# Optimization experiments

Hardware: AMD Instinct MI355X
Metric: run time of the kernel (lower is better)

Reference implementation:

```python
import jax, jax.numpy as jnp
import numpy as np

# --- low precision float format: exp=5, man=2, subnormals, nearest-even ---
EXP, MAN = 5, 2
BIAS = 2 ** (EXP - 1) - 1          # 15
EMIN = 1 - BIAS                     # -14 (min normal exponent; clamping here gives subnormals)
MAXV = (2.0 - 2.0 ** (-MAN)) * 2.0 ** BIAS


def _q(x):
    """Round x to nearest FP(exp=5, man=2) value (subnormals, clipped at max)."""
    ax = jnp.abs(x)
    e = jnp.floor(jnp.log2(jnp.where(ax > 0, ax, 1.0)))
    e = jnp.maximum(e, EMIN)
    scale = jnp.exp2(e - MAN)
    q = jnp.round(x / scale) * scale   # jnp.round = half-to-even
    q = jnp.clip(q, -MAXV, MAXV)
    return jnp.where(ax > 0, q, x).astype(x.dtype)


# Quantizer: forward quantize, straight-through (quantized) backward
@jax.custom_vjp
def fq(x):
    return _q(x)

def _fq_fwd(x):
    return _q(x), None

def _fq_bwd(_, g):
    return (_q(g),)

fq.defvjp(_fq_fwd, _fq_bwd)


def conv_valid(x, w):
    return jax.lax.conv_general_dilated(
        x, w, window_strides=(1, 1), padding='VALID',
        dimension_numbers=('NCHW', 'OIHW', 'NCHW'))


def qconv(x, w):
    # QConv2d: input_quant, weight_quant, conv, output_quant
    return fq(conv_valid(fq(x), fq(w)))


def qlinear(x, W, b):
    # QLinear: input_quant, weight_quant (weights + bias), matmul, output_quant
    return fq(fq(x) @ fq(W).T + fq(b))


def batchnorm(x, gamma, beta, eps=1e-5):
    # training-mode BatchNorm2d over (N,H,W) per channel
    m = x.mean(axis=(0, 2, 3), keepdims=True)
    v = x.var(axis=(0, 2, 3), keepdims=True)
    return (x - m) * jax.lax.rsqrt(v + eps) * gamma[None, :, None, None] + beta[None, :, None, None]


def maxpool2(x):
    return jax.lax.reduce_window(x, -jnp.inf, jax.lax.max,
                                 (1, 1, 2, 2), (1, 1, 2, 2), 'VALID')


def setup_inputs() -> dict:
    key = jax.random.key(0)
    ks = jax.random.split(key, 12)
    B = 8192
    inp = {
        'x':   jax.random.normal(ks[0], (B, 1, 32, 32), jnp.float32),
        'w1':  jax.random.normal(ks[1], (6, 1, 5, 5), jnp.float32) * 0.2,
        'g1':  jnp.ones((6,), jnp.float32),
        'be1': jnp.zeros((6,), jnp.float32),
        'w2':  jax.random.normal(ks[2], (16, 6, 5, 5), jnp.float32) * 0.1,
        'g2':  jnp.ones((16,), jnp.float32),
        'be2': jnp.zeros((16,), jnp.float32),
        'fw1': jax.random.normal(ks[3], (120, 400), jnp.float32) * 0.05,
        'fb1': jnp.zeros((120,), jnp.float32),
        'fw2': jax.random.normal(ks[4], (84, 120), jnp.float32) * 0.09,
        'fb2': jnp.zeros((84,), jnp.float32),
        'fw3': jax.random.normal(ks[5], (10, 84), jnp.float32) * 0.1,
        'fb3': jnp.zeros((10,), jnp.float32),
    }
    return inp


def reference(x, w1, g1, be1, w2, g2, be2, fw1, fb1, fw2, fb2, fw3, fb3):
    x = fq(x)                                   # act_error_quant
    x = qconv(x, w1)                            # conv1 (no bias)
    x = batchnorm(x, g1, be1)                   # bn1
    x = fq(x)                                   # act_error_quant
    x = maxpool2(jax.nn.relu(x))                # relu + 2x2 maxpool -> [B,6,14,14]
    x = qconv(x, w2)                            # conv2 -> [B,16,10,10]
    x = batchnorm(x, g2, be2)                   # bn2
    x = fq(x)
    x = maxpool2(jax.nn.relu(x))                # -> [B,16,5,5]
    x = x.reshape(x.shape[0], -1)               # [B,400]
    x = jax.nn.relu(qlinear(x, fw1, fb1))       # fc1
    x = jax.nn.relu(qlinear(x, fw2, fb2))       # fc2
    x = qlinear(x, fw3, fb3)                    # fc3 -> [B,10]
    return x
```

## Files before the change

### kernel.cpp

```cpp
#include <hip/hip_runtime.h>
#include <hip/hip_bf16.h>


#define BATCH 8192

__device__ __forceinline__ double fq_d(double x) {
    long long b = __double_as_longlong(x);
    long long ab = b & 0x7fffffffffffffffLL;
    if (ab == 0) return x;
    double q;
    if (ab >= 0x3F10000000000000LL) {
        long long r = b + 0x0001FFFFFFFFFFFFLL + ((b >> 50) & 1LL);
        r &= 0xFFFC000000000000LL;
        q = __longlong_as_double(r);
        q = fmin(fmax(q, -57344.0), 57344.0);
    } else {
        q = rint(x * 65536.0) * 1.52587890625e-05;
    }
    return q;
}

__device__ __forceinline__ float fq_f(float x) {
    int b = __float_as_int(x);
    int ab = b & 0x7fffffff;
    if (ab == 0) return x;
    float q;
    if (ab >= 0x38800000) {
        int r = b + 0x000FFFFF + ((b >> 21) & 1);
        r &= 0xFFE00000;
        q = __int_as_float(r);
        q = fminf(fmaxf(q, -57344.0f), 57344.0f);
    } else {
        q = rintf(x * 65536.0f) * 1.52587890625e-05f;
    }
    return q;
}

__device__ __forceinline__ unsigned short bfbits(double q) {
    __hip_bfloat16 h = __float2bfloat16((float)q);
    return *(unsigned short*)&h;
}

__global__ void kprep(const float* __restrict__ w1, const float* __restrict__ w2,
                      const float* __restrict__ fb1, const float* __restrict__ fb2,
                      const float* __restrict__ fb3, const float* __restrict__ fw1,
                      const float* __restrict__ fw2, const float* __restrict__ fw3,
                      float* __restrict__ qw1, float* __restrict__ qw2,
                      float* __restrict__ qfb1, float* __restrict__ qfb2,
                      float* __restrict__ qfb3, float* __restrict__ Wt1,
                      float* __restrict__ Wt2, float* __restrict__ Wt3) {
    int i = blockIdx.x * 256 + threadIdx.x;
    if (i < 150) { qw1[i] = fq_f(w1[i]); return; }
    i -= 150;
    if (i < 2400) { qw2[i] = fq_f(w2[i]); return; }
    i -= 2400;
    if (i < 120) { qfb1[i] = fq_f(fb1[i]); return; }
    i -= 120;
    if (i < 84) { qfb2[i] = fq_f(fb2[i]); return; }
    i -= 84;
    if (i < 10) { qfb3[i] = fq_f(fb3[i]); return; }
    i -= 10;
    if (i < 51200) { int k = i / 128, o = i % 128;
        Wt1[i] = (o < 120) ? fq_f(fw1[o * 400 + k]) : 0.0f; return; }
    i -= 51200;
    if (i < 15360) { int k = i / 128, o = i % 128;
        Wt2[i] = (o < 84) ? fq_f(fw2[o * 120 + k]) : 0.0f; return; }
    i -= 15360;
    if (i < 1344) { int k = i / 16, o = i % 16;
        Wt3[i] = (o < 10) ? fq_f(fw3[o * 84 + k]) : 0.0f; return; }
}
#define PREP_TOTAL (150 + 2400 + 120 + 84 + 10 + 51200 + 15360 + 1344)

__global__ __launch_bounds__(256) void kconv1(const float* __restrict__ x,
        const float* __restrict__ qw, __hip_bfloat16* __restrict__ c1,
        int nimg_total, double* __restrict__ st1) {
    __shared__ float sxf[3 * 1056];
    __shared__ double swd[152];
    __shared__ double sred[6][2];
    int t = threadIdx.x;
    int b0 = blockIdx.x * 3;
    int nimg = nimg_total - b0; if (nimg > 3) nimg = 3;
    for (int i = t; i < nimg * 1024; i += 256) {
        int img = i >> 10, idx = i & 1023;
        sxf[img * 1056 + (idx >> 5) * 33 + (idx & 31)] =
            fq_f(x[(size_t)(b0 + img) * 1024 + idx]);
    }
    if (t < 150) swd[t] = (double)qw[t];
    if (t >= 192 && t < 204) ((double*)sred)[t - 192] = 0.0;
    __syncthreads();
    int ntask = nimg * 336;
    for (int task = t; task < ntask; task += 256) {
        int img = task / 336; int rr = task % 336;
        int co = rr / 56; int rem = rr % 56;
        int i0 = (rem >> 2) * 2;
        int j0 = (rem & 3) * 7;
        const double* wp = &swd[co * 25];
        double a0[7], a1[7];
        #pragma unroll
        for (int j = 0; j < 7; ++j) { a0[j] = 0.0; a1[j] = 0.0; }
        double wr[5], wq[5];
        #pragma unroll
        for (int u = 0; u < 6; ++u) {
            const float* xr = &sxf[img * 1056 + (i0 + u) * 33 + j0];
            double xv[11];
            #pragma unroll
            for (int k = 0; k < 11; ++k) xv[k] = (double)xr[k];
            if (u < 5) {
                #pragma unroll
                for (int tt = 0; tt < 5; ++tt) wr[tt] = wp[u * 5 + tt];
                #pragma unroll
                for (int j = 0; j < 7; ++j)
                    a0[j] = fma(xv[j], wr[0], fma(xv[j+1], wr[1], fma(xv[j+2], wr[2],
                            fma(xv[j+3], wr[3], fma(xv[j+4], wr[4], a0[j])))));
            }
            if (u >= 1) {
                #pragma unroll
                for (int j = 0; j < 7; ++j)
                    a1[j] = fma(xv[j], wq[0], fma(xv[j+1], wq[1], fma(xv[j+2], wq[2],
                            fma(xv[j+3], wq[3], fma(xv[j+4], wq[4], a1[j])))));
            }
            #pragma unroll
            for (int tt = 0; tt < 5; ++tt) wq[tt] = wr[tt];
        }
        size_t base = ((size_t)(b0 + img) * 6 + co) * 784 + (size_t)i0 * 28 + j0;
        double s = 0.0, s2 = 0.0;
        #pragma unroll
        for (int j = 0; j < 7; ++j) {
            double q0 = fq_d(a0[j]), q1 = fq_d(a1[j]);
            ((unsigned short*)c1)[base + j]      = bfbits(q0);
            ((unsigned short*)c1)[base + 28 + j] = bfbits(q1);
            s += q0 + q1; s2 += q0 * q0 + q1 * q1;
        }
        atomicAdd(&sred[co][0], s);
        atomicAdd(&sred[co][1], s2);
    }
    __syncthreads();
    if (t < 12) atomicAdd(&st1[t * 32 + (blockIdx.x & 31)], ((double*)sred)[t]);
}

__global__ void kfinal(const double* __restrict__ st, double* __restrict__ mr,
                       int C, double N) {
    int c = threadIdx.x;
    if (c < C) {
        double s = 0.0, s2 = 0.0;
        for (int b = 0; b < 32; ++b) { s += st[c * 64 + b]; s2 += st[c * 64 + 32 + b]; }
        double m = s / N;
        double v = s2 / N - m * m;
        mr[2 * c] = m;
        mr[2 * c + 1] = 1.0 / sqrt(v + 1e-5);
    }
}

__global__ __launch_bounds__(256) void kpool1(const __hip_bfloat16* __restrict__ c1,
        const double* __restrict__ mr1, const float* __restrict__ g1,
        const float* __restrict__ be1, __hip_bfloat16* __restrict__ p1) {
    int idx = blockIdx.x * 256 + threadIdx.x;
    int pp = idx % 7;  int t1 = idx / 7;
    int ph = t1 % 14;  int t2 = t1 / 14;
    int c  = t2 % 6;   int b  = t2 / 6;
    double m = mr1[2 * c], r = mr1[2 * c + 1];
    double gg = (double)g1[c], bb = (double)be1[c];
    bool useMax = (r * gg) >= 0.0;
    const __hip_bfloat16* src = c1 + (((size_t)b * 6 + c) * 28 + 2 * ph) * 28 + 4 * pp;
    ushort4 u0 = *(const ushort4*)src;
    ushort4 u1 = *(const ushort4*)(src + 28);
    float f0 = __bfloat162float(*(__hip_bfloat16*)&u0.x), f1 = __bfloat162float(*(__hip_bfloat16*)&u0.y);
    float f2 = __bfloat162float(*(__hip_bfloat16*)&u0.z), f3 = __bfloat162float(*(__hip_bfloat16*)&u0.w);
    float f4 = __bfloat162float(*(__hip_bfloat16*)&u1.x), f5 = __bfloat162float(*(__hip_bfloat16*)&u1.y);
    float f6 = __bfloat162float(*(__hip_bfloat16*)&u1.z), f7 = __bfloat162float(*(__hip_bfloat16*)&u1.w);
    float va = useMax ? fmaxf(fmaxf(f0, f1), fmaxf(f4, f5))
                      : fminf(fminf(f0, f1), fminf(f4, f5));
    float vb = useMax ? fmaxf(fmaxf(f2, f3), fmaxf(f6, f7))
                      : fminf(fminf(f2, f3), fminf(f6, f7));
    double qa = fq_d((((double)va - m) * r) * gg + bb);
    double qb = fq_d((((double)vb - m) * r) * gg + bb);
    qa = fmax(qa, 0.0); qb = fmax(qb, 0.0);
    ushort2 pk; pk.x = bfbits(qa); pk.y = bfbits(qb);
    *(ushort2*)&p1[((size_t)b * 6 + c) * 196 + ph * 14 + 2 * pp] = pk;
}

__global__ __launch_bounds__(320) void kconv2(const __hip_bfloat16* __restrict__ p1,
        const float* __restrict__ qw, __hip_bfloat16* __restrict__ c2,
        double* __restrict__ st2) {
    __shared__ float sxf[4704];
    __shared__ float swf[2400];
    __shared__ double sred[16][2];
    int t = threadIdx.x;
    int b0 = blockIdx.x * 4;
    for (int i = t; i < 4704; i += 320) sxf[i] = __bfloat162float(p1[(size_t)b0 * 1176 + i]);
    for (int i = t; i < 2400; i += 320) swf[i] = qw[i];
    if (t < 32) ((double*)sred)[t] = 0.0;
    __syncthreads();
    int img = t / 80, r = t % 80;
    int co = r / 5, i0 = (r % 5) * 2;
    const float* xb = &sxf[img * 1176];
    const float* wb = &swf[co * 150];
    double a0[10], a1[10];
    #pragma unroll
    for (int j = 0; j < 10; ++j) { a0[j] = 0.0; a1[j] = 0.0; }
    double wr[5], wq[5];
    for (int ci = 0; ci < 6; ++ci) {
        #pragma unroll
        for (int u = 0; u < 6; ++u) {
            const float* xr = &xb[ci * 196 + (i0 + u) * 14];
            double xv[14];
            #pragma unroll
            for (int k = 0; k < 14; ++k) xv[k] = (double)xr[k];
            if (u < 5) {
                #pragma unroll
                for (int tt = 0; tt < 5; ++tt) wr[tt] = (double)wb[ci * 25 + u * 5 + tt];
                #pragma unroll
                for (int j = 0; j < 10; ++j)
                    a0[j] = fma(xv[j], wr[0], fma(xv[j+1], wr[1], fma(xv[j+2], wr[2],
                            fma(xv[j+3], wr[3], fma(xv[j+4], wr[4], a0[j])))));
            }
            if (u >= 1) {
                #pragma unroll
                for (int j = 0; j < 10; ++j)
                    a1[j] = fma(xv[j], wq[0], fma(xv[j+1], wq[1], fma(xv[j+2], wq[2],
                            fma(xv[j+3], wq[3], fma(xv[j+4], wq[4], a1[j])))));
            }
            #pragma unroll
            for (int tt = 0; tt < 5; ++tt) wq[tt] = wr[tt];
        }
    }
    size_t base = ((size_t)(b0 + img) * 16 + co) * 100 + (size_t)i0 * 10;
    double s = 0.0, s2 = 0.0;
    #pragma unroll
    for (int j = 0; j < 10; ++j) {
        double q0 = fq_d(a0[j]), q1 = fq_d(a1[j]);
        ((unsigned short*)c2)[base + j]      = bfbits(q0);
        ((unsigned short*)c2)[base + 10 + j] = bfbits(q1);
        s += q0 + q1; s2 += q0 * q0 + q1 * q1;
    }
    atomicAdd(&sred[co][0], s);
    atomicAdd(&sred[co][1], s2);
    __syncthreads();
    if (t < 32) atomicAdd(&st2[t * 32 + (blockIdx.x & 31)], ((double*)sred)[t]);
}

__global__ __launch_bounds__(256) void kfc1(const __hip_bfloat16* __restrict__ c2,
        const double* __restrict__ st2, const float* __restrict__ g2,
        const float* __restrict__ be2, const float* __restrict__ Wt,
        const float* __restrict__ qb, __hip_bfloat16* __restrict__ outb) {
    constexpr int IN = 400, OUT = 120, OUTP = 128, ROWS = 4, BT = 8;
    __shared__ double sx[BT][IN];
    __shared__ double sbn[16][4];
    int t = threadIdx.x;
    int b0 = blockIdx.x * BT;
    if (t < 16) {
        double s = 0.0, s2 = 0.0;
        for (int b = 0; b < 32; ++b) { s += st2[t * 64 + b]; s2 += st2[t * 64 + 32 + b]; }
        double m = s / (819200.0);
        double v = s2 / (819200.0) - m * m;
        sbn[t][0] = m; sbn[t][1] = 1.0 / sqrt(v + 1e-5);
        sbn[t][2] = (double)g2[t]; sbn[t][3] = (double)be2[t];
    }
    __syncthreads();
    for (int i = t; i < BT * IN; i += 256) {
        int r = i / IN, k = i % IN;
        int c = k / 25, rem = k % 25;
        int ph = rem / 5, pw = rem % 5;
        const __hip_bfloat16* src = c2 + (((size_t)(b0 + r) * 16 + c) * 10 + 2 * ph) * 10 + 2 * pw;
        double m = sbn[c][0], rr = sbn[c][1], gg = sbn[c][2], bb = sbn[c][3];
        float f0 = __bfloat162float(src[0]),  f1 = __bfloat162float(src[1]);
        float f2 = __bfloat162float(src[10]), f3 = __bfloat162float(src[11]);
        bool useMax = (rr * gg) >= 0.0;
        float v = useMax ? fmaxf(fmaxf(f0, f1), fmaxf(f2, f3))
                         : fminf(fminf(f0, f1), fminf(f2, f3));
        double q = fq_d((((double)v - m) * rr) * gg + bb);
        sx[r][k] = fmax(q, 0.0);
    }
    __syncthreads();
    int o = t % OUTP;
    int g = t / OUTP;
    double acc[ROWS];
    double bias = (o < OUT) ? (double)qb[o] : 0.0;
    #pragma unroll
    for (int r = 0; r < ROWS; ++r) acc[r] = bias;
    #pragma unroll 4
    for (int k = 0; k < IN; ++k) {
        double w = (double)Wt[k * OUTP + o];
        #pragma unroll
        for (int r = 0; r < ROWS; ++r)
            acc[r] = fma(sx[g * ROWS + r][k], w, acc[r]);
    }
    if (o < OUT) {
        #pragma unroll
        for (int r = 0; r < ROWS; ++r) {
            double q = fq_d(acc[r]);
            if (q < 0.0) q = 0.0;
            outb[(size_t)(b0 + g * ROWS + r) * OUT + o] = __float2bfloat16((float)q);
        }
    }
}

__global__ __launch_bounds__(256) void kfc23(const __hip_bfloat16* __restrict__ a1,
        const float* __restrict__ Wt2, const float* __restrict__ qfb2,
        const float* __restrict__ Wt3, const float* __restrict__ qfb3,
        float* __restrict__ out) {
    __shared__ double sx1[16][120];
    __shared__ double s2[16][84];
    int t = threadIdx.x;
    int b0 = blockIdx.x * 16;
    for (int i = t; i < 16 * 120; i += 256) {
        int r = i / 120, k = i % 120;
        sx1[r][k] = (double)__bfloat162float(a1[(size_t)(b0 + r) * 120 + k]);
    }
    __syncthreads();
    {
        int o = t % 128, g = t / 128;
        double acc[8];
        double bias = (o < 84) ? (double)qfb2[o] : 0.0;
        #pragma unroll
        for (int r = 0; r < 8; ++r) acc[r] = bias;
        #pragma unroll 4
        for (int k = 0; k < 120; ++k) {
            double w = (double)Wt2[k * 128 + o];
            #pragma unroll
            for (int r = 0; r < 8; ++r)
                acc[r] = fma(sx1[g * 8 + r][k], w, acc[r]);
        }
        if (o < 84) {
            #pragma unroll
            for (int r = 0; r < 8; ++r) {
                double q = fq_d(acc[r]);
                s2[g * 8 + r][o] = fmax(q, 0.0);
            }
        }
    }
    __syncthreads();
    {
        int o = t % 16, g = t / 16;
        double acc = (o < 10) ? (double)qfb3[o] : 0.0;
        #pragma unroll 4
        for (int k = 0; k < 84; ++k)
            acc = fma(s2[g][k], (double)Wt3[k * 16 + o], acc);
        if (o < 10)
            out[(size_t)(b0 + g) * 10 + o] = (float)fq_d(acc);
    }
}

extern "C" void kernel_launch(void* const* d_in, const int* in_sizes, int n_in,
                              void* d_out, int out_size, void* d_ws, size_t ws_size,
                              hipStream_t stream) {
    const float* x   = (const float*)d_in[0];
    const float* w1  = (const float*)d_in[1];
    const float* g1  = (const float*)d_in[2];
    const float* be1 = (const float*)d_in[3];
    const float* w2  = (const float*)d_in[4];
    const float* g2  = (const float*)d_in[5];
    const float* be2 = (const float*)d_in[6];
    const float* fw1 = (const float*)d_in[7];
    const float* fb1 = (const float*)d_in[8];
    const float* fw2 = (const float*)d_in[9];
    const float* fb2 = (const float*)d_in[10];
    const float* fw3 = (const float*)d_in[11];
    const float* fb3 = (const float*)d_in[12];

    char* ws = (char*)d_ws;
    double* stats1 = (double*)(ws + 0);
    double* stats2 = (double*)(ws + 3072);
    double* mr1    = (double*)(ws + 11264);
    float* qw1  = (float*)(ws + 12288);
    float* qw2  = (float*)(ws + 13312);
    float* qfb1 = (float*)(ws + 23040);
    float* qfb2 = (float*)(ws + 23552);
    float* qfb3 = (float*)(ws + 24064);
    float* Wt1  = (float*)(ws + 24576);
    float* Wt2  = (float*)(ws + 229376);
    float* Wt3  = (float*)(ws + 290816);
    __hip_bfloat16* c1 = (__hip_bfloat16*)(ws + 303104);
    __hip_bfloat16* p1 = (__hip_bfloat16*)(ws + 77373440);
    __hip_bfloat16* c2 = (__hip_bfloat16*)(ws + 303104);
    __hip_bfloat16* a1 = (__hip_bfloat16*)(ws + 303104 + 26214400);

    hipMemsetAsync(ws, 0, 11264, stream);

    kprep<<<(PREP_TOTAL + 255) / 256, 256, 0, stream>>>(
        w1, w2, fb1, fb2, fb3, fw1, fw2, fw3,
        qw1, qw2, qfb1, qfb2, qfb3, Wt1, Wt2, Wt3);

    kconv1<<<(BATCH + 2) / 3, 256, 0, stream>>>(x, qw1, c1, BATCH, stats1);
    kfinal<<<1, 32, 0, stream>>>(stats1, mr1, 6, (double)BATCH * 784.0);
    kpool1<<<BATCH * 6 * 14 * 7 / 256, 256, 0, stream>>>(c1, mr1, g1, be1, p1);
    kconv2<<<BATCH / 4, 320, 0, stream>>>(p1, qw2, c2, stats2);
    kfc1<<<BATCH / 8, 256, 0, stream>>>(c2, stats2, g2, be2, Wt1, qfb1, a1);
    kfc23<<<BATCH / 16, 256, 0, stream>>>(a1, Wt2, qfb2, Wt3, qfb3, (float*)d_out);
}
```

Before: 412.1 us.

## Run conv2 as implicit GEMM on FP64 MFMA with channel-last output layout

```diff
diff --git a/kernel.cpp b/kernel.cpp
--- a/kernel.cpp
+++ b/kernel.cpp
@@ -3,6 +3,8 @@
 
 
 #define BATCH 8192
+
+typedef double d4 __attribute__((ext_vector_type(4)));
 
 __device__ __forceinline__ double fq_d(double x) {
     long long b = __double_as_longlong(x);
@@ -182,59 +184,69 @@
 __global__ __launch_bounds__(320) void kconv2(const __hip_bfloat16* __restrict__ p1,
         const float* __restrict__ qw, __hip_bfloat16* __restrict__ c2,
         double* __restrict__ st2) {
-    __shared__ float sxf[4704];
-    __shared__ float swf[2400];
+    __shared__ float sxf[9408];
+    __shared__ double swd[2432];
+    __shared__ int soff[152];
     __shared__ double sred[16][2];
     int t = threadIdx.x;
-    int b0 = blockIdx.x * 4;
-    for (int i = t; i < 4704; i += 320) sxf[i] = __bfloat162float(p1[(size_t)b0 * 1176 + i]);
-    for (int i = t; i < 2400; i += 320) swf[i] = qw[i];
+    int b0 = blockIdx.x * 8;
+    const ushort4* srcp = (const ushort4*)(p1 + (size_t)b0 * 1176);
+    for (int i = t; i < 2352; i += 320) {
+        ushort4 u = srcp[i];
+        float* d = &sxf[4 * i];
+        d[0] = __bfloat162float(*(__hip_bfloat16*)&u.x);
+        d[1] = __bfloat162float(*(__hip_bfloat16*)&u.y);
+        d[2] = __bfloat162float(*(__hip_bfloat16*)&u.z);
+        d[3] = __bfloat162float(*(__hip_bfloat16*)&u.w);
+    }
+    for (int i = t; i < 2432; i += 320) {
+        int k = i >> 4, co = i & 15;
+        swd[i] = (k < 150) ? (double)qw[co * 150 + k] : 0.0;
+    }
+    if (t < 152) {
+        int k = t;
+        soff[k] = (k < 150) ? (k / 25) * 196 + ((k % 25) / 5) * 14 + (k % 5) : 0;
+    }
     if (t < 32) ((double*)sred)[t] = 0.0;
     __syncthreads();
-    int img = t / 80, r = t % 80;
-    int co = r / 5, i0 = (r % 5) * 2;
-    const float* xb = &sxf[img * 1176];
-    const float* wb = &swf[co * 150];
-    double a0[10], a1[10];
+
+    int l = t & 63, w = t >> 6;
+    int c = l >> 4, r16 = l & 15;
+
+    d4 pz = {0.0, 0.0, 0.0, 0.0};
+    d4 prow = __builtin_amdgcn_mfma_f64_16x16x4f64((double)r16, 0.25, pz, 0, 0, 0);
+    d4 pcol = __builtin_amdgcn_mfma_f64_16x16x4f64(1.0, 0.25 * (double)r16, pz, 0, 0, 0);
+    int rowidx[4], colidx[4];
     #pragma unroll
-    for (int j = 0; j < 10; ++j) { a0[j] = 0.0; a1[j] = 0.0; }
-    double wr[5], wq[5];
-    for (int ci = 0; ci < 6; ++ci) {
-        #pragma unroll
-        for (int u = 0; u < 6; ++u) {
-            const float* xr = &xb[ci * 196 + (i0 + u) * 14];
-            double xv[14];
-            #pragma unroll
-            for (int k = 0; k < 14; ++k) xv[k] = (double)xr[k];
-            if (u < 5) {
-                #pragma unroll
-                for (int tt = 0; tt < 5; ++tt) wr[tt] = (double)wb[ci * 25 + u * 5 + tt];
-                #pragma unroll
-                for (int j = 0; j < 10; ++j)
-                    a0[j] = fma(xv[j], wr[0], fma(xv[j+1], wr[1], fma(xv[j+2], wr[2],
-                            fma(xv[j+3], wr[3], fma(xv[j+4], wr[4], a0[j])))));
-            }
-            if (u >= 1) {
-                #pragma unroll
-                for (int j = 0; j < 10; ++j)
-                    a1[j] = fma(xv[j], wq[0], fma(xv[j+1], wq[1], fma(xv[j+2], wq[2],
-                            fma(xv[j+3], wq[3], fma(xv[j+4], wq[4], a1[j])))));
-            }
-            #pragma unroll
-            for (int tt = 0; tt < 5; ++tt) wq[tt] = wr[tt];
-        }
-    }
-    size_t base = ((size_t)(b0 + img) * 16 + co) * 100 + (size_t)i0 * 10;
-    double s = 0.0, s2 = 0.0;
+    for (int j = 0; j < 4; ++j) { rowidx[j] = (int)prow[j]; colidx[j] = (int)pcol[j]; }
+
+    double bw[38];
     #pragma unroll
-    for (int j = 0; j < 10; ++j) {
-        double q0 = fq_d(a0[j]), q1 = fq_d(a1[j]);
-        ((unsigned short*)c2)[base + j]      = bfbits(q0);
-        ((unsigned short*)c2)[base + 10 + j] = bfbits(q1);
-        s += q0 + q1; s2 += q0 * q0 + q1 * q1;
-    }
-    atomicAdd(&sred[co][0], s);
-    atomicAdd(&sred[co][1], s2);
+    for (int s = 0; s < 38; ++s) bw[s] = swd[(4 * s + c) * 16 + r16];
+
+    double ls = 0.0, ls2 = 0.0;
+    int co0 = colidx[0];
+    for (int tile = w; tile < 50; tile += 5) {
+        int pos = tile * 16 + r16;
+        int img = pos / 100, pp = pos % 100;
+        int abase = img * 1176 + (pp / 10) * 14 + (pp % 10);
+        d4 acc = {0.0, 0.0, 0.0, 0.0};
+        #pragma unroll
+        for (int s = 0; s < 38; ++s) {
+            double av = (double)sxf[abase + soff[4 * s + c]];
+            acc = __builtin_amdgcn_mfma_f64_16x16x4f64(av, bw[s], acc, 0, 0, 0);
+        }
+        #pragma unroll
+        for (int j = 0; j < 4; ++j) {
+            int po = tile * 16 + rowidx[j];
+            int im2 = po / 100, pq = po % 100;
+            double q = fq_d(acc[j]);
+            ((unsigned short*)c2)[((size_t)(b0 + im2) * 100 + pq) * 16 + colidx[j]] = bfbits(q);
+            ls += q; ls2 += q * q;
+        }
+    }
+    atomicAdd(&sred[co0][0], ls);
+    atomicAdd(&sred[co0][1], ls2);
     __syncthreads();
     if (t < 32) atomicAdd(&st2[t * 32 + (blockIdx.x & 31)], ((double*)sred)[t]);
 }
@@ -261,10 +273,10 @@
         int r = i / IN, k = i % IN;
         int c = k / 25, rem = k % 25;
         int ph = rem / 5, pw = rem % 5;
-        const __hip_bfloat16* src = c2 + (((size_t)(b0 + r) * 16 + c) * 10 + 2 * ph) * 10 + 2 * pw;
+        const __hip_bfloat16* src = c2 + ((size_t)(b0 + r) * 100 + 20 * ph + 2 * pw) * 16 + c;
         double m = sbn[c][0], rr = sbn[c][1], gg = sbn[c][2], bb = sbn[c][3];
-        float f0 = __bfloat162float(src[0]),  f1 = __bfloat162float(src[1]);
-        float f2 = __bfloat162float(src[10]), f3 = __bfloat162float(src[11]);
+        float f0 = __bfloat162float(src[0]),   f1 = __bfloat162float(src[16]);
+        float f2 = __bfloat162float(src[160]), f3 = __bfloat162float(src[176]);
         bool useMax = (rr * gg) >= 0.0;
         float v = useMax ? fmaxf(fmaxf(f0, f1), fmaxf(f2, f3))
                          : fminf(fminf(f0, f1), fminf(f2, f3));
@@ -384,7 +396,7 @@
     kconv1<<<(BATCH + 2) / 3, 256, 0, stream>>>(x, qw1, c1, BATCH, stats1);
     kfinal<<<1, 32, 0, stream>>>(stats1, mr1, 6, (double)BATCH * 784.0);
     kpool1<<<BATCH * 6 * 14 * 7 / 256, 256, 0, stream>>>(c1, mr1, g1, be1, p1);
-    kconv2<<<BATCH / 4, 320, 0, stream>>>(p1, qw2, c2, stats2);
+    kconv2<<<BATCH / 8, 320, 0, stream>>>(p1, qw2, c2, stats2);
     kfc1<<<BATCH / 8, 256, 0, stream>>>(c2, stats2, g2, be2, Wt1, qfb1, a1);
     kfc23<<<BATCH / 16, 256, 0, stream>>>(a1, Wt2, qfb2, Wt3, qfb3, (float*)d_out);
 }
```

Result: slower. 437.1 us (+6.1%).
